# Optimization experiments

Measured on AMD Instinct MI355X. Metric: run time of the kernel, lower is better.

The kernel has to match this reference:

```python
import jax, jax.numpy as jnp
import numpy as np

H = 256          # hidden_size
W2V = 256        # word2vec embedding dim
FEAT = 4096      # video frame feature dim
T_ENC = 80       # video_frame


def _lstm_cell(x, h, c, W_ih, W_hh, b_ih, b_hh):
    # PyTorch LSTMCell gate order: i, f, g, o
    gates = x @ W_ih.T + b_ih + h @ W_hh.T + b_hh
    i, f, g, o = jnp.split(gates, 4, axis=-1)
    c_new = jax.nn.sigmoid(f) * c + jax.nn.sigmoid(i) * jnp.tanh(g)
    h_new = jax.nn.sigmoid(o) * jnp.tanh(c_new)
    return h_new, c_new


def setup_inputs() -> dict:
    key = jax.random.key(0)
    ks = jax.random.split(key, 14)
    B, L, V = 256, 40, 6000
    sc = 0.02
    inp = {
        "feat": jax.random.normal(ks[0], (B, T_ENC, FEAT), jnp.float32),
        "caption": jax.random.normal(ks[1], (B, L, W2V), jnp.float32),
        "caption_one_hot": jax.random.normal(ks[2], (B, L, V), jnp.float32),
        # lstm1: input 4096 -> hidden 256
        "W_ih1": jax.random.normal(ks[3], (4 * H, FEAT), jnp.float32) * sc,
        "W_hh1": jax.random.normal(ks[4], (4 * H, H), jnp.float32) * sc,
        "b_ih1": jnp.zeros((4 * H,), jnp.float32),
        "b_hh1": jnp.zeros((4 * H,), jnp.float32),
        # lstm2: input hidden+word2vec = 512 -> hidden 256
        "W_ih2": jax.random.normal(ks[5], (4 * H, H + W2V), jnp.float32) * sc,
        "W_hh2": jax.random.normal(ks[6], (4 * H, H), jnp.float32) * sc,
        "b_ih2": jnp.zeros((4 * H,), jnp.float32),
        "b_hh2": jnp.zeros((4 * H,), jnp.float32),
        # output projection hidden -> vocab
        "W_out": jax.random.normal(ks[7], (V, H), jnp.float32) * sc,
        "b_out": jnp.zeros((V,), jnp.float32),
    }
    return inp


def reference(feat, caption, caption_one_hot,
              W_ih1, W_hh1, b_ih1, b_hh1,
              W_ih2, W_hh2, b_ih2, b_hh2,
              W_out, b_out):
    B = feat.shape[0]
    L = caption.shape[1]  # decoder_length
    pad1 = jnp.zeros((B, FEAT), feat.dtype)
    pad2 = jnp.zeros((B, H), feat.dtype)
    h1 = jnp.zeros((B, H), feat.dtype)
    c1 = jnp.zeros((B, H), feat.dtype)
    h2 = jnp.zeros((B, H), feat.dtype)
    c2 = jnp.zeros((B, H), feat.dtype)

    # ---- encoding phase: 80 video frames ----
    def enc_step(carry, x_t):
        h1, c1, h2, c2 = carry
        h1, c1 = _lstm_cell(x_t, h1, c1, W_ih1, W_hh1, b_ih1, b_hh1)
        h2, c2 = _lstm_cell(jnp.concatenate([pad2, h1], axis=1), h2, c2,
                            W_ih2, W_hh2, b_ih2, b_hh2)
        return (h1, c1, h2, c2), None

    carry, _ = jax.lax.scan(enc_step, (h1, c1, h2, c2),
                            feat.transpose(1, 0, 2))  # [T,B,4096]

    # ---- decoding phase: decoder_length-1 steps with per-step CE ----
    targets = jnp.argmax(caption_one_hot, axis=-1)      # [B,L] int
    dec_in = caption[:, :L - 1, :].transpose(1, 0, 2)   # [L-1,B,W2V]
    dec_tgt = targets[:, 1:].T                          # [L-1,B]

    def dec_step(carry, xt):
        h1, c1, h2, c2 = carry
        cap_t, tgt_t = xt
        h1, c1 = _lstm_cell(pad1, h1, c1, W_ih1, W_hh1, b_ih1, b_hh1)
        h2, c2 = _lstm_cell(jnp.concatenate([cap_t, h1], axis=1), h2, c2,
                            W_ih2, W_hh2, b_ih2, b_hh2)
        logits = h2 @ W_out.T + b_out                   # [B,V]
        lsm = jax.nn.log_softmax(logits, axis=-1)
        nll = -jnp.take_along_axis(lsm, tgt_t[:, None], axis=1)[:, 0]
        # torch: total_loss += sum(word_loss)/batch_size  ==  mean over batch
        return (h1, c1, h2, c2), jnp.mean(nll)

    _, step_losses = jax.lax.scan(dec_step, carry, (dec_in, dec_tgt))
    return jnp.sum(step_losses)
```

## Files before the change

kernel.cpp:

```cpp
#include <hip/hip_runtime.h>


typedef unsigned short u16;
typedef unsigned int u32;
typedef unsigned long long u64;
typedef __attribute__((ext_vector_type(8))) short s8v;
typedef __attribute__((ext_vector_type(4))) float f4v;

#define VOC   6000
#define VOCP  6144
#define HSTR  65536

__device__ __forceinline__ u16 f2b(float f) {
  unsigned u = __float_as_uint(f);
  return (u16)((u + 0x7fffu + ((u >> 16) & 1u)) >> 16);
}
__device__ __forceinline__ float b2f(u16 u) { return __uint_as_float(((unsigned)u) << 16); }
__device__ __forceinline__ float sigm(float x) { return 1.f / (1.f + __expf(-x)); }
__device__ __forceinline__ float tanh_f(float x) {
  float e = __expf(-2.f * fabsf(x));
  float t = (1.f - e) / (1.f + e);
  return x >= 0.f ? t : -t;
}

__global__ __launch_bounds__(256) void conv_tr(const float* __restrict__ src,
                                               u16* __restrict__ dst, int T, int D, int toff) {
  const int tl = blockIdx.x >> 8, b = blockIdx.x & 255;
  const float* s = src + ((size_t)b * T + toff + tl) * D;
  u16* d = dst + (size_t)blockIdx.x * D;
  for (int i = threadIdx.x * 8; i < D; i += 2048) {
    float4 a = *(const float4*)(s + i);
    float4 c = *(const float4*)(s + i + 4);
    unsigned w0 = (unsigned)f2b(a.x) | ((unsigned)f2b(a.y) << 16);
    unsigned w1 = (unsigned)f2b(a.z) | ((unsigned)f2b(a.w) << 16);
    unsigned w2 = (unsigned)f2b(c.x) | ((unsigned)f2b(c.y) << 16);
    unsigned w3 = (unsigned)f2b(c.z) | ((unsigned)f2b(c.w) << 16);
    *(int4*)(d + i) = make_int4((int)w0, (int)w1, (int)w2, (int)w3);
  }
}

__global__ void pack_bf16(u16* __restrict__ dst, int dld, int doff,
                          const float* __restrict__ src, int sld, int soff,
                          int Wc, int R, int Rsrc) {
  int i = blockIdx.x * 256 + threadIdx.x;
  if (i >= Wc * R) return;
  int r = i / Wc, c = i - r * Wc;
  float v = (r < Rsrc) ? src[(size_t)r * sld + soff + c] : 0.f;
  dst[(size_t)r * dld + doff + c] = f2b(v);
}

__global__ void bias_setup(const float* __restrict__ bi1, const float* __restrict__ bh1,
                           const float* __restrict__ bi2, const float* __restrict__ bh2,
                           const float* __restrict__ bo,
                           float* __restrict__ b1s, float* __restrict__ b2s,
                           float* __restrict__ bop) {
  int i = blockIdx.x * 256 + threadIdx.x;
  if (i < 1024) { b1s[i] = bi1[i] + bh1[i]; b2s[i] = bi2[i] + bh2[i]; }
  if (i < VOCP) bop[i] = (i < VOC) ? bo[i] : -1e30f;
}

__global__ __launch_bounds__(256) void argmax_kernel(const float* __restrict__ coh,
                                                     int* __restrict__ tgt) {
  const int d = blockIdx.x >> 8;
  const int b = blockIdx.x & 255;
  const float4* row = (const float4*)(coh + ((size_t)b * 40 + (d + 1)) * VOC);
  float best = -3.4e38f; int bi = 0;
  for (int v = threadIdx.x; v < VOC / 4; v += 256) {
    float4 x = row[v];
    float vals[4] = {x.x, x.y, x.z, x.w};
#pragma unroll
    for (int j = 0; j < 4; ++j)
      if (vals[j] > best) { best = vals[j]; bi = v * 4 + j; }
  }
#pragma unroll
  for (int o = 1; o < 64; o <<= 1) {
    float ov = __shfl_xor(best, o);
    int   oi = __shfl_xor(bi, o);
    if (ov > best || (ov == best && oi < bi)) { best = ov; bi = oi; }
  }
  __shared__ float sv[4]; __shared__ int si[4];
  if ((threadIdx.x & 63) == 0) { sv[threadIdx.x >> 6] = best; si[threadIdx.x >> 6] = bi; }
  __syncthreads();
  if (threadIdx.x == 0) {
    for (int i = 1; i < 4; ++i)
      if (sv[i] > best || (sv[i] == best && si[i] < bi)) { best = sv[i]; bi = si[i]; }
    tgt[blockIdx.x] = bi;
  }
}

template <int MODE>
__global__ __launch_bounds__(256) void gemm_bb(
    const u16* __restrict__ A, const u16* __restrict__ Bw,
    const float* __restrict__ bias, void* __restrict__ out0,
    float* __restrict__ ps, float* __restrict__ tgtlog, const int* __restrict__ tgt,
    int K, int moff)
{
  int mt, nt;
  if (MODE == 0) {
    const int xcd = (int)blockIdx.x & 7;
    nt = xcd & 3;
    mt = (xcd >> 2) * 40 + ((int)blockIdx.x >> 3);
  } else {
    mt = (int)blockIdx.x / 24;
    nt = (int)blockIdx.x % 24;
  }
  const int m0 = mt * 128;
  const int n0 = nt * 256;
  const int tid = threadIdx.x;
  const int lane = tid & 63;
  const int wid = tid >> 6;
  const int wm = wid >> 1, wn = wid & 1;
  const int fr = lane & 15;
  const int fk = (lane >> 4) * 8;
  const int rq = lane >> 4;

  __shared__ u16 As[128][72];
  __shared__ u16 Bs[256][72];
  f4v acc[4][8] = {};

  const int ar = tid >> 1, ac = (tid & 1) * 32;
  int4 av[4], bv[8];
  {
    const u16* ap = A + (size_t)(m0 + ar) * K + ac;
    const u16* bp = Bw + (size_t)(n0 + tid) * K;
#pragma unroll
    for (int v = 0; v < 4; ++v) av[v] = *(const int4*)(ap + v * 8);
#pragma unroll
    for (int v = 0; v < 8; ++v) bv[v] = *(const int4*)(bp + v * 8);
  }
#pragma unroll 1
  for (int k0 = 0; k0 < K; k0 += 64) {
    __syncthreads();
#pragma unroll
    for (int v = 0; v < 4; ++v) *(int4*)&As[ar][ac + v * 8] = av[v];
#pragma unroll
    for (int v = 0; v < 8; ++v) *(int4*)&Bs[tid][v * 8] = bv[v];
    __syncthreads();
    if (k0 + 64 < K) {
      const u16* ap = A + (size_t)(m0 + ar) * K + k0 + 64 + ac;
      const u16* bp = Bw + (size_t)(n0 + tid) * K + k0 + 64;
#pragma unroll
      for (int v = 0; v < 4; ++v) av[v] = *(const int4*)(ap + v * 8);
#pragma unroll
      for (int v = 0; v < 8; ++v) bv[v] = *(const int4*)(bp + v * 8);
    }
#pragma unroll
    for (int ks = 0; ks < 2; ++ks) {
      const int kb = ks * 32 + fk;
      s8v a[4], b[8];
#pragma unroll
      for (int i = 0; i < 4; ++i) a[i] = *(const s8v*)&As[wm * 64 + i * 16 + fr][kb];
#pragma unroll
      for (int j = 0; j < 8; ++j) b[j] = *(const s8v*)&Bs[wn * 128 + j * 16 + fr][kb];
#pragma unroll
      for (int i = 0; i < 4; ++i)
#pragma unroll
        for (int j = 0; j < 8; ++j)
          acc[i][j] = __builtin_amdgcn_mfma_f32_16x16x32_bf16(a[i], b[j], acc[i][j], 0, 0, 0);
    }
  }

  float bz[8];
#pragma unroll
  for (int j = 0; j < 8; ++j) bz[j] = bias[n0 + wn * 128 + j * 16 + fr];

  if (MODE == 2) {
    const int tile = nt * 2 + wn;
    float* pm = (float*)out0;
#pragma unroll
    for (int i = 0; i < 4; ++i) {
#pragma unroll
      for (int r = 0; r < 4; ++r) {
        const int row = m0 + wm * 64 + i * 16 + rq * 4 + r;
        const int tg = tgt[row];
        float vj[8]; float m = -1e30f;
#pragma unroll
        for (int j = 0; j < 8; ++j) {
          const int n = n0 + wn * 128 + j * 16 + fr;
          float v = acc[i][j][r] + bz[j];
          vj[j] = v;
          m = fmaxf(m, v);
          if (n == tg) tgtlog[row] = v;
        }
#pragma unroll
        for (int o = 1; o < 16; o <<= 1) m = fmaxf(m, __shfl_xor(m, o));
        float s = 0.f;
#pragma unroll
        for (int j = 0; j < 8; ++j) s += __expf(vj[j] - m);
#pragma unroll
        for (int o = 1; o < 16; o <<= 1) s += __shfl_xor(s, o);
        if (fr == 0) { pm[(size_t)row * 48 + tile] = m; ps[(size_t)row * 48 + tile] = s; }
      }
    }
  } else {
    u16* X = (u16*)out0;
#pragma unroll
    for (int i = 0; i < 4; ++i)
#pragma unroll
      for (int r = 0; r < 4; ++r) {
        const int row = moff + m0 + wm * 64 + i * 16 + rq * 4 + r;
        u16* crow = X + (size_t)row * 1024;
#pragma unroll
        for (int j = 0; j < 8; ++j)
          crow[n0 + wn * 128 + j * 16 + fr] = f2b(acc[i][j][r] + bz[j]);
      }
  }
}

__global__ __launch_bounds__(128, 1) void recur_kernel(
    const u16* __restrict__ X1t,
    const u16* __restrict__ Xct,
    const float* __restrict__ b1sum, const float* __restrict__ b2sum,
    const u16* __restrict__ Whh1,
    const u16* __restrict__ Wcat2,
    u16* __restrict__ h1hist,
    u16* __restrict__ h2hist,
    u32* __restrict__ f1, u32* __restrict__ f2)
{
  __shared__ u16 wlds[64 * 512];
  const int tid = threadIdx.x;
  const int lane = tid & 63;
  const int w = tid >> 6;
  const int fr = lane & 15;
  const int fk8 = lane >> 4;
  const int fk = fk8 * 8;
  const int rq = lane >> 4;
  const bool p2 = blockIdx.x >= 64;
  const int bb = p2 ? (int)blockIdx.x - 64 : (int)blockIdx.x;
  const int bm = bb >> 4;
  const int bh = bb & 15;
  const int hd = bh * 16 + fr;
  const int LD = p2 ? 512 : 256;
  const int C8m = (p2 ? 64 : 32) - 1;
  const int KK = p2 ? 16 : 8;

  {
    const u16* Wsrc = p2 ? Wcat2 : Whh1;
    const int C8 = C8m + 1;
    for (int idx = tid; idx < 64 * C8; idx += 128) {
      int l = idx / C8, c8 = idx - l * C8;
      int gr = (l >> 4) * 256 + bh * 16 + (l & 15);
      int4 v = *(const int4*)(Wsrc + (size_t)gr * LD + c8 * 8);
      *(int4*)&wlds[l * LD + (((c8 + 4 * l) & C8m) * 8)] = v;
    }
  }
  float br4[4];
  {
    const float* bsrc = p2 ? b2sum : b1sum;
#pragma unroll
    for (int q = 0; q < 4; ++q) br4[q] = bsrc[q * 256 + hd];
  }
  __syncthreads();

  float creg[2][4] = {};
  u32* myflag = (p2 ? f2 : f1) + bm * 16 + bh;

#pragma unroll 1
  for (int s = 0; s < 119; ++s) {
    const u16* Xb = nullptr;
    if (!p2 && s < 80)  Xb = X1t + (size_t)s * 262144;
    if (p2  && s >= 80) Xb = Xct + (size_t)(s - 80) * 262144;
    float ga[2][4][4];
    if (Xb) {
#pragma unroll
      for (int i = 0; i < 2; ++i)
#pragma unroll
        for (int r = 0; r < 4; ++r) {
          const int bat = bm * 64 + w * 32 + i * 16 + rq * 4 + r;
          const u16* xp = Xb + (size_t)bat * 1024;
#pragma unroll
          for (int q = 0; q < 4; ++q) ga[i][r][q] = b2f(xp[q * 256 + hd]);
        }
    } else {
#pragma unroll
      for (int i = 0; i < 2; ++i)
#pragma unroll
        for (int r = 0; r < 4; ++r)
#pragma unroll
          for (int q = 0; q < 4; ++q) ga[i][r][q] = br4[q];
    }
    if (p2 || s > 0) {
      const u32 tA = p2 ? (u32)(s + 1) : (u32)s;
      const u32 tB = (u32)s;
      while (true) {
        bool ok = true;
        if (lane < 16)
          ok = __hip_atomic_load(&f1[bm * 16 + lane], __ATOMIC_RELAXED,
                                 __HIP_MEMORY_SCOPE_AGENT) >= tA;
        else if (p2 && lane < 32)
          ok = __hip_atomic_load(&f2[bm * 16 + (lane - 16)], __ATOMIC_RELAXED,
                                 __HIP_MEMORY_SCOPE_AGENT) >= tB;
        if (__all(ok)) break;
        __builtin_amdgcn_s_sleep(1);
      }
    }
    const u16* h1base = h1hist + (size_t)(p2 ? s + 1 : s) * HSTR;
    const u16* h2base = h2hist + (size_t)s * HSTR;
    s8v a[2][16];
#pragma unroll
    for (int i = 0; i < 2; ++i) {
      const int row = bm * 64 + w * 32 + i * 16 + fr;
#pragma unroll
      for (int kk = 0; kk < 16; ++kk) {
        if (kk < KK) {
          const u16* src = (kk < 8) ? (h1base + (size_t)row * 256 + kk * 32 + fk)
                                    : (h2base + (size_t)row * 256 + (kk - 8) * 32 + fk);
          union { u64 q[2]; s8v v; } u;
          u.q[0] = __hip_atomic_load((const u64*)src,     __ATOMIC_RELAXED,
                                     __HIP_MEMORY_SCOPE_AGENT);
          u.q[1] = __hip_atomic_load((const u64*)src + 1, __ATOMIC_RELAXED,
                                     __HIP_MEMORY_SCOPE_AGENT);
          a[i][kk] = u.v;
        }
      }
    }
    f4v acc[2][4] = {};
#pragma unroll
    for (int kk = 0; kk < 16; ++kk) {
      if (kk < KK) {
#pragma unroll
        for (int q = 0; q < 4; ++q) {
          const int l = q * 16 + fr;
          s8v b = *(const s8v*)&wlds[l * LD + (((kk * 4 + fk8 + 4 * l) & C8m) * 8)];
#pragma unroll
          for (int i = 0; i < 2; ++i)
            acc[i][q] = __builtin_amdgcn_mfma_f32_16x16x32_bf16(a[i][kk], b, acc[i][q], 0, 0, 0);
        }
      }
    }
    u16* hwbase = (p2 ? h2hist : h1hist) + (size_t)(s + 1) * HSTR;
#pragma unroll
    for (int i = 0; i < 2; ++i) {
#pragma unroll
      for (int r = 0; r < 4; ++r) {
        const int bat = bm * 64 + w * 32 + i * 16 + rq * 4 + r;
        float g0 = acc[i][0][r] + ga[i][r][0], g1 = acc[i][1][r] + ga[i][r][1];
        float g2 = acc[i][2][r] + ga[i][r][2], g3 = acc[i][3][r] + ga[i][r][3];
        float cn = sigm(g1) * creg[i][r] + sigm(g0) * tanh_f(g2);
        float h = sigm(g3) * tanh_f(cn);
        creg[i][r] = cn;
        unsigned hb = f2b(h);
        unsigned ob = (unsigned)__shfl_xor((int)hb, 1);
        if ((fr & 1) == 0)
          __hip_atomic_store((u32*)(hwbase + (size_t)bat * 256 + hd), hb | (ob << 16),
                             __ATOMIC_RELAXED, __HIP_MEMORY_SCOPE_AGENT);
      }
    }
    asm volatile("s_waitcnt vmcnt(0)" ::: "memory");
    __syncthreads();
    if (tid == 0)
      __hip_atomic_store(myflag, (u32)(s + 1), __ATOMIC_RELAXED, __HIP_MEMORY_SCOPE_AGENT);
  }
}

__global__ __launch_bounds__(256) void nll_combine(const float* __restrict__ pm,
                                                   const float* __restrict__ ps,
                                                   const float* __restrict__ tgtlog,
                                                   float* __restrict__ rowloss) {
  int row = blockIdx.x * 256 + threadIdx.x;
  if (row >= 9984) return;
  const float* pmr = pm + (size_t)row * 48;
  const float* psr = ps + (size_t)row * 48;
  float M = -1e30f;
#pragma unroll
  for (int t = 0; t < 48; ++t) M = fmaxf(M, pmr[t]);
  float S = 0.f;
#pragma unroll
  for (int t = 0; t < 48; ++t) S += psr[t] * __expf(pmr[t] - M);
  rowloss[row] = M + __logf(S) - tgtlog[row];
}

__global__ __launch_bounds__(256) void final_kernel(const float* __restrict__ rowloss,
                                                    float* __restrict__ out) {
  float s = 0.f;
  for (int n = threadIdx.x; n < 9984; n += 256) s += rowloss[n];
#pragma unroll
  for (int o = 1; o < 64; o <<= 1) s += __shfl_xor(s, o);
  __shared__ float sr[4];
  if ((threadIdx.x & 63) == 0) sr[threadIdx.x >> 6] = s;
  __syncthreads();
  if (threadIdx.x == 0) out[0] = (sr[0] + sr[1] + sr[2] + sr[3]) * (1.f / 256.f);
}

extern "C" void kernel_launch(void* const* d_in, const int* in_sizes, int n_in,
                              void* d_out, int out_size, void* d_ws, size_t ws_size,
                              hipStream_t stream) {
  const float* feat    = (const float*)d_in[0];
  const float* caption = (const float*)d_in[1];
  const float* coh     = (const float*)d_in[2];
  const float* W_ih1   = (const float*)d_in[3];
  const float* W_hh1   = (const float*)d_in[4];
  const float* b_ih1   = (const float*)d_in[5];
  const float* b_hh1   = (const float*)d_in[6];
  const float* W_ih2   = (const float*)d_in[7];
  const float* W_hh2   = (const float*)d_in[8];
  const float* b_ih2   = (const float*)d_in[9];
  const float* b_hh2   = (const float*)d_in[10];
  const float* W_out   = (const float*)d_in[11];
  const float* b_out   = (const float*)d_in[12];

  char* p = (char*)d_ws;
  auto take = [&](size_t bytes) { char* r = p; p += (bytes + 255) & ~(size_t)255; return r; };
  u16* X1t    = (u16*)take(80ull * 256 * 1024 * 2);
  u16* Xct    = (u16*)take(40ull * 256 * 1024 * 2);
  u16* h1hist = (u16*)take(120ull * HSTR * 2);
  u16* h2hist = (u16*)take(120ull * HSTR * 2);
  u16* Wih1b  = (u16*)take(1024ull * 4096 * 2);
  u16* Whh1b  = (u16*)take(1024ull * 256 * 2);
  u16* Wih2ab = (u16*)take(1024ull * 256 * 2);
  u16* Wcat2b = (u16*)take(1024ull * 512 * 2);
  u16* Woutb  = (u16*)take((size_t)VOCP * 256 * 2);
  float* b1sum = (float*)take(1024 * 4);
  float* b2sum = (float*)take(1024 * 4);
  float* boutp = (float*)take(VOCP * 4);
  int*   tgt   = (int*)take(9984 * 4);
  float* tgtlog = (float*)take(9984 * 4);
  float* pm    = (float*)take(9984ull * 48 * 4);
  float* ps    = (float*)take(9984ull * 48 * 4);
  float* rowloss = (float*)take(9984 * 4);
  u32* f1      = (u32*)take(256);
  u32* f2      = (u32*)take(256);
  char* uni = take(10240ull * 4096 * 2);
  u16* capT  = (u16*)uni;
  u16* featT = (u16*)uni;

  hipMemsetAsync(h1hist, 0, HSTR * 2, stream);
  hipMemsetAsync(h2hist, 0, HSTR * 2, stream);
  hipMemsetAsync(f1, 0, 512, stream);

  bias_setup<<<dim3(24), dim3(256), 0, stream>>>(b_ih1, b_hh1, b_ih2, b_hh2, b_out,
                                                 b1sum, b2sum, boutp);
  auto pack = [&](u16* dst, int dld, int doff, const float* src, int sld, int soff,
                  int Wc, int R, int Rs) {
    int tot = Wc * R;
    pack_bf16<<<dim3((tot + 255) / 256), dim3(256), 0, stream>>>(dst, dld, doff, src, sld, soff,
                                                                 Wc, R, Rs);
  };
  pack(Wih1b, 4096, 0, W_ih1, 4096, 0, 4096, 1024, 1024);
  pack(Whh1b, 256, 0, W_hh1, 256, 0, 256, 1024, 1024);
  pack(Wih2ab, 256, 0, W_ih2, 512, 0, 256, 1024, 1024);
  pack(Wcat2b, 512, 0, W_ih2, 512, 256, 256, 1024, 1024);
  pack(Wcat2b, 512, 256, W_hh2, 256, 0, 256, 1024, 1024);
  pack(Woutb, 256, 0, W_out, 256, 0, 256, VOCP, VOC);

  argmax_kernel<<<dim3(39 * 256), dim3(256), 0, stream>>>(coh, tgt);

  conv_tr<<<dim3(10240), dim3(256), 0, stream>>>(caption, capT, 40, 256, 0);
  gemm_bb<0><<<dim3(320), dim3(256), 0, stream>>>(capT, Wih2ab, b2sum, Xct,
                                                  nullptr, nullptr, nullptr, 256, 0);

  for (int c = 0; c < 2; ++c) {
    conv_tr<<<dim3(10240), dim3(256), 0, stream>>>(feat, featT, 80, 4096, c * 40);
    gemm_bb<0><<<dim3(320), dim3(256), 0, stream>>>(featT, Wih1b, b1sum, X1t,
                                                    nullptr, nullptr, nullptr, 4096,
                                                    c * 10240);
  }

  recur_kernel<<<dim3(128), dim3(128), 0, stream>>>(X1t, Xct, b1sum, b2sum,
                                                    Whh1b, Wcat2b, h1hist, h2hist, f1, f2);

  gemm_bb<2><<<dim3(1872), dim3(256), 0, stream>>>(h2hist + 81ull * HSTR, Woutb, boutp, pm,
                                                   ps, tgtlog, tgt, 256, 0);
  nll_combine<<<dim3(39), dim3(256), 0, stream>>>(pm, ps, tgtlog, rowloss);
  final_kernel<<<dim3(1), dim3(256), 0, stream>>>(rowloss, (float*)d_out);
}
```

Measured before the change: 2.471 ms.

## Fuse input-projection GEMM into persistent recurrence kernel with per-step readiness counters

Replaces the separate feature transpose and input-projection GEMM launches with extra blocks inside one persistent kernel. Those blocks read fp32 features directly, convert them to bf16 on the fly, and publish each timestep's projection through an atomic counter. The recurrence blocks wait on that counter, so the big encoder GEMM can overlap with the serial LSTM steps and the featT transpose buffer is no longer needed. The risks are a possible deadlock if the 512 blocks are not all co-resident, slower direct fp32 loads from the strided feature layout, and contention between GEMM blocks and the latency-bound recurrence.

Result: slower. 3.021 ms (+22.3%).

```diff
diff --git a/kernel.cpp b/kernel.cpp
--- a/kernel.cpp
+++ b/kernel.cpp
@@ -207,26 +207,123 @@
   }
 }
 
-__global__ __launch_bounds__(128, 1) void recur_kernel(
-    const u16* __restrict__ X1t,
+__global__ __launch_bounds__(256, 1) void mega_kernel(
+    const float* __restrict__ feat,
     const u16* __restrict__ Xct,
     const float* __restrict__ b1sum, const float* __restrict__ b2sum,
+    const u16* __restrict__ Wih1b,
     const u16* __restrict__ Whh1,
     const u16* __restrict__ Wcat2,
-    u16* __restrict__ h1hist,
-    u16* __restrict__ h2hist,
-    u32* __restrict__ f1, u32* __restrict__ f2)
+    u16* __restrict__ X1t,
+    u16* __restrict__ h1hist, u16* __restrict__ h2hist,
+    u32* __restrict__ f1, u32* __restrict__ f2, u32* __restrict__ xcnt)
 {
-  __shared__ u16 wlds[64 * 512];
+  __shared__ u16 smem[32768];
+  const int bid = blockIdx.x;
   const int tid = threadIdx.x;
+
+  if (bid >= 128) {
+    u16 (*As)[72] = (u16 (*)[72])smem;
+    u16 (*Bs)[72] = (u16 (*)[72])(smem + 128 * 72);
+    const int wk = bid - 128;
+    const int lane = tid & 63, wid = tid >> 6;
+    const int wm = wid >> 1, wn = wid & 1;
+    const int fr = lane & 15, fk = (lane >> 4) * 8, rq = lane >> 4;
+    const int ar = tid >> 1, acol = (tid & 1) * 32;
+#pragma unroll 1
+    for (int tl = wk; tl < 640; tl += 384) {
+      const int t = tl >> 3, mh = (tl >> 2) & 1, nt = tl & 3;
+      const int n0 = nt * 256;
+      const float* Af = feat + ((size_t)(mh * 128 + ar) * 80 + t) * 4096 + acol;
+      const u16* Bp = Wih1b + (size_t)(n0 + tid) * 4096;
+      f4v acc[4][8] = {};
+      float av[32]; int4 bv[8];
+#pragma unroll
+      for (int v = 0; v < 8; ++v) {
+        float4 t4 = *(const float4*)(Af + v * 4);
+        av[v*4+0] = t4.x; av[v*4+1] = t4.y; av[v*4+2] = t4.z; av[v*4+3] = t4.w;
+      }
+#pragma unroll
+      for (int v = 0; v < 8; ++v) bv[v] = *(const int4*)(Bp + v * 8);
+#pragma unroll 1
+      for (int k0 = 0; k0 < 4096; k0 += 64) {
+        __syncthreads();
+#pragma unroll
+        for (int v = 0; v < 4; ++v) {
+          unsigned w0 = (unsigned)f2b(av[v*8+0]) | ((unsigned)f2b(av[v*8+1]) << 16);
+          unsigned w1 = (unsigned)f2b(av[v*8+2]) | ((unsigned)f2b(av[v*8+3]) << 16);
+          unsigned w2 = (unsigned)f2b(av[v*8+4]) | ((unsigned)f2b(av[v*8+5]) << 16);
+          unsigned w3 = (unsigned)f2b(av[v*8+6]) | ((unsigned)f2b(av[v*8+7]) << 16);
+          *(int4*)&As[ar][acol + v * 8] = make_int4((int)w0, (int)w1, (int)w2, (int)w3);
+        }
+#pragma unroll
+        for (int v = 0; v < 8; ++v) *(int4*)&Bs[tid][v * 8] = bv[v];
+        __syncthreads();
+        if (k0 + 64 < 4096) {
+#pragma unroll
+          for (int v = 0; v < 8; ++v) {
+            float4 t4 = *(const float4*)(Af + k0 + 64 + v * 4);
+            av[v*4+0] = t4.x; av[v*4+1] = t4.y; av[v*4+2] = t4.z; av[v*4+3] = t4.w;
+          }
+#pragma unroll
+          for (int v = 0; v < 8; ++v) bv[v] = *(const int4*)(Bp + k0 + 64 + v * 8);
+        }
+#pragma unroll
+        for (int ks = 0; ks < 2; ++ks) {
+          const int kb = ks * 32 + fk;
+          s8v a[4], b[8];
+#pragma unroll
+          for (int i = 0; i < 4; ++i) a[i] = *(const s8v*)&As[wm * 64 + i * 16 + fr][kb];
+#pragma unroll
+          for (int j = 0; j < 8; ++j) b[j] = *(const s8v*)&Bs[wn * 128 + j * 16 + fr][kb];
+#pragma unroll
+          for (int i = 0; i < 4; ++i)
+#pragma unroll
+            for (int j = 0; j < 8; ++j)
+              acc[i][j] = __builtin_amdgcn_mfma_f32_16x16x32_bf16(a[i], b[j], acc[i][j], 0, 0, 0);
+        }
+      }
+      float bz[8];
+#pragma unroll
+      for (int j = 0; j < 8; ++j) bz[j] = b1sum[n0 + wn * 128 + j * 16 + fr];
+      const size_t rowbase = (size_t)t * 256 + mh * 128;
+#pragma unroll
+      for (int i = 0; i < 4; ++i)
+#pragma unroll
+        for (int r = 0; r < 4; ++r) {
+          u16* crow = X1t + (rowbase + wm * 64 + i * 16 + rq * 4 + r) * 1024;
+#pragma unroll
+          for (int j = 0; j < 8; ++j) {
+            const int n = n0 + wn * 128 + j * 16 + fr;
+            u32 hb = f2b(acc[i][j][r] + bz[j]);
+            u32 ob = (u32)__shfl_xor((int)hb, 1);
+            if (!(lane & 1))
+              __hip_atomic_store((u32*)(crow + n), hb | (ob << 16),
+                                 __ATOMIC_RELAXED, __HIP_MEMORY_SCOPE_AGENT);
+          }
+        }
+      asm volatile("s_waitcnt vmcnt(0)" ::: "memory");
+      __syncthreads();
+      if (tid == 0)
+        __hip_atomic_fetch_add(&xcnt[t], 1u, __ATOMIC_RELAXED, __HIP_MEMORY_SCOPE_AGENT);
+    }
+    return;
+  }
+
+  if (tid >= 128) {
+    __syncthreads();
+    for (int s = 0; s < 119; ++s) __syncthreads();
+    return;
+  }
+  u16* wlds = smem;
   const int lane = tid & 63;
   const int w = tid >> 6;
   const int fr = lane & 15;
   const int fk8 = lane >> 4;
   const int fk = fk8 * 8;
   const int rq = lane >> 4;
-  const bool p2 = blockIdx.x >= 64;
-  const int bb = p2 ? (int)blockIdx.x - 64 : (int)blockIdx.x;
+  const bool p2 = bid >= 64;
+  const int bb = p2 ? bid - 64 : bid;
   const int bm = bb >> 4;
   const int bh = bb & 15;
   const int hd = bh * 16 + fr;
@@ -257,39 +354,48 @@
 
 #pragma unroll 1
   for (int s = 0; s < 119; ++s) {
-    const u16* Xb = nullptr;
-    if (!p2 && s < 80)  Xb = X1t + (size_t)s * 262144;
-    if (p2  && s >= 80) Xb = Xct + (size_t)(s - 80) * 262144;
     float ga[2][4][4];
-    if (Xb) {
-#pragma unroll
-      for (int i = 0; i < 2; ++i)
-#pragma unroll
-        for (int r = 0; r < 4; ++r) {
-          const int bat = bm * 64 + w * 32 + i * 16 + rq * 4 + r;
-          const u16* xp = Xb + (size_t)bat * 1024;
-#pragma unroll
-          for (int q = 0; q < 4; ++q) ga[i][r][q] = b2f(xp[q * 256 + hd]);
-        }
+    if (p2) {
+      if (s >= 80) {
+        const u16* Xb = Xct + (size_t)(s - 80) * 262144;
+#pragma unroll
+        for (int i = 0; i < 2; ++i)
+#pragma unroll
+          for (int r = 0; r < 4; ++r) {
+            const int bat = bm * 64 + w * 32 + i * 16 + rq * 4 + r;
+            const u16* xp = Xb + (size_t)bat * 1024;
+#pragma unroll
+            for (int q = 0; q < 4; ++q) ga[i][r][q] = b2f(xp[q * 256 + hd]);
+          }
+      } else {
+#pragma unroll
+        for (int i = 0; i < 2; ++i)
+#pragma unroll
+          for (int r = 0; r < 4; ++r)
+#pragma unroll
+            for (int q = 0; q < 4; ++q) ga[i][r][q] = br4[q];
+      }
+      {
+        const u32 tA = (u32)(s + 1), tB = (u32)s;
+        while (true) {
+          bool ok = true;
+          if (lane < 16)
+            ok = __hip_atomic_load(&f1[bm * 16 + lane], __ATOMIC_RELAXED,
+                                   __HIP_MEMORY_SCOPE_AGENT) >= tA;
+          else if (lane < 32)
+            ok = __hip_atomic_load(&f2[bm * 16 + (lane - 16)], __ATOMIC_RELAXED,
+                                   __HIP_MEMORY_SCOPE_AGENT) >= tB;
+          if (__all(ok)) break;
+          __builtin_amdgcn_s_sleep(1);
+        }
+      }
     } else {
-#pragma unroll
-      for (int i = 0; i < 2; ++i)
-#pragma unroll
-        for (int r = 0; r < 4; ++r)
-#pragma unroll
-          for (int q = 0; q < 4; ++q) ga[i][r][q] = br4[q];
-    }
-    if (p2 || s > 0) {
-      const u32 tA = p2 ? (u32)(s + 1) : (u32)s;
-      const u32 tB = (u32)s;
       while (true) {
         bool ok = true;
-        if (lane < 16)
-          ok = __hip_atomic_load(&f1[bm * 16 + lane], __ATOMIC_RELAXED,
-                                 __HIP_MEMORY_SCOPE_AGENT) >= tA;
-        else if (p2 && lane < 32)
-          ok = __hip_atomic_load(&f2[bm * 16 + (lane - 16)], __ATOMIC_RELAXED,
-                                 __HIP_MEMORY_SCOPE_AGENT) >= tB;
+        if (lane < 16) { if (s > 0) ok = __hip_atomic_load(&f1[bm * 16 + lane],
+                             __ATOMIC_RELAXED, __HIP_MEMORY_SCOPE_AGENT) >= (u32)s; }
+        else if (lane == 16) { if (s < 80) ok = __hip_atomic_load(&xcnt[s],
+                             __ATOMIC_RELAXED, __HIP_MEMORY_SCOPE_AGENT) >= 8u; }
         if (__all(ok)) break;
         __builtin_amdgcn_s_sleep(1);
       }
@@ -312,6 +418,34 @@
                                      __HIP_MEMORY_SCOPE_AGENT);
           a[i][kk] = u.v;
         }
+      }
+    }
+    if (!p2) {
+      if (s < 80) {
+        const u16* Xb = X1t + (size_t)s * 262144;
+#pragma unroll
+        for (int i = 0; i < 2; ++i)
+#pragma unroll
+          for (int r = 0; r < 4; ++r) {
+            const int bat = bm * 64 + w * 32 + i * 16 + rq * 4 + r;
+            const u32* xp = (const u32*)(Xb + (size_t)bat * 1024);
+#pragma unroll
+            for (int q = 0; q < 4; ++q) {
+              u32 wv = 0;
+              if (!(lane & 1))
+                wv = __hip_atomic_load(&xp[(q * 256 + hd) >> 1], __ATOMIC_RELAXED,
+                                       __HIP_MEMORY_SCOPE_AGENT);
+              u32 ov = (u32)__shfl_xor((int)wv, 1);
+              ga[i][r][q] = b2f((lane & 1) ? (u16)(ov >> 16) : (u16)wv);
+            }
+          }
+      } else {
+#pragma unroll
+        for (int i = 0; i < 2; ++i)
+#pragma unroll
+          for (int r = 0; r < 4; ++r)
+#pragma unroll
+            for (int q = 0; q < 4; ++q) ga[i][r][q] = br4[q];
       }
     }
     f4v acc[2][4] = {};
@@ -410,6 +544,7 @@
   u16* Wih2ab = (u16*)take(1024ull * 256 * 2);
   u16* Wcat2b = (u16*)take(1024ull * 512 * 2);
   u16* Woutb  = (u16*)take((size_t)VOCP * 256 * 2);
+  u16* capT   = (u16*)take(10240ull * 256 * 2);
   float* b1sum = (float*)take(1024 * 4);
   float* b2sum = (float*)take(1024 * 4);
   float* boutp = (float*)take(VOCP * 4);
@@ -420,13 +555,12 @@
   float* rowloss = (float*)take(9984 * 4);
   u32* f1      = (u32*)take(256);
   u32* f2      = (u32*)take(256);
-  char* uni = take(10240ull * 4096 * 2);
-  u16* capT  = (u16*)uni;
-  u16* featT = (u16*)uni;
+  u32* xcnt    = (u32*)take(512);
 
   hipMemsetAsync(h1hist, 0, HSTR * 2, stream);
   hipMemsetAsync(h2hist, 0, HSTR * 2, stream);
   hipMemsetAsync(f1, 0, 512, stream);
+  hipMemsetAsync(xcnt, 0, 512, stream);
 
   bias_setup<<<dim3(24), dim3(256), 0, stream>>>(b_ih1, b_hh1, b_ih2, b_hh2, b_out,
                                                  b1sum, b2sum, boutp);
@@ -449,15 +583,9 @@
   gemm_bb<0><<<dim3(320), dim3(256), 0, stream>>>(capT, Wih2ab, b2sum, Xct,
                                                   nullptr, nullptr, nullptr, 256, 0);
 
-  for (int c = 0; c < 2; ++c) {
-    conv_tr<<<dim3(10240), dim3(256), 0, stream>>>(feat, featT, 80, 4096, c * 40);
-    gemm_bb<0><<<dim3(320), dim3(256), 0, stream>>>(featT, Wih1b, b1sum, X1t,
-                                                    nullptr, nullptr, nullptr, 4096,
-                                                    c * 10240);
-  }
-
-  recur_kernel<<<dim3(128), dim3(128), 0, stream>>>(X1t, Xct, b1sum, b2sum,
-                                                    Whh1b, Wcat2b, h1hist, h2hist, f1, f2);
+  mega_kernel<<<dim3(512), dim3(256), 0, stream>>>(feat, Xct, b1sum, b2sum,
+                                                   Wih1b, Whh1b, Wcat2b,
+                                                   X1t, h1hist, h2hist, f1, f2, xcnt);
 
   gemm_bb<2><<<dim3(1872), dim3(256), 0, stream>>>(h2hist + 81ull * HSTR, Woutb, boutp, pm,
                                                    ps, tgtlog, tgt, 256, 0);
```
